# Optimization experiments

Measured on AMD Instinct MI355X. Metric: run time of the kernel, lower is better.

The kernel has to match this reference:

```python
import jax, jax.numpy as jnp
import numpy as np

N, D, K = 131072, 64, 4096


def setup_inputs() -> dict:
    key = jax.random.key(0)
    k1, k2 = jax.random.split(key)
    x = jax.random.normal(k1, (N, D), dtype=jnp.float32)
    embed = jax.random.normal(k2, (K, D), dtype=jnp.float32)
    return {"x": x, "embed": embed}


def reference(x, embed):
    """EuclideanCodebook forward.

    x:     [N, D] flat input vectors
    embed: [K, D] codebook
    Returns (quantize [N,D], embed_ind [N], cluster_size [K], embed_sum [K,D]).
    cluster_size / embed_sum are the one-hot scatter statistics fed to the
    EMA codebook update (embed_onehot.sum(0) and flatten^T @ embed_onehot).
    """
    num_codes = embed.shape[0]
    x2 = jnp.sum(x * x, axis=-1, keepdims=True)               # [N, 1]
    e2 = jnp.sum(embed * embed, axis=-1)                      # [K]
    dist = x2 - 2.0 * (x @ embed.T) + e2[None, :]             # [N, K]
    embed_ind = jnp.argmin(dist, axis=-1)                     # [N]
    quantize = embed[embed_ind]                               # gather [N, D]
    # scatter statistics for EMA update
    cluster_size = jnp.zeros((num_codes,), x.dtype).at[embed_ind].add(1.0)  # [K]
    embed_sum = jax.ops.segment_sum(x, embed_ind, num_segments=num_codes)   # [K, D]
    return quantize, embed_ind, cluster_size, embed_sum
```

## Files before the change

kernel.cpp:

```cpp
#include <hip/hip_runtime.h>

#define N_ROWS 131072
#define DIM 64
#define K_CODES 4096
#define BROWS 256
#define CK 64
#define NCH (K_CODES / CK)
#define EST 72
#define EPS 0.015625f
#define HEPS 0.0078125f

typedef __attribute__((ext_vector_type(8))) short short8;
typedef __attribute__((ext_vector_type(4))) float f32x4;

__device__ inline unsigned short bf16rn(float f) {
    unsigned int u = __float_as_uint(f);
    u += 0x7FFFu + ((u >> 16) & 1u);
    return (unsigned short)(u >> 16);
}
__device__ inline unsigned int fkey(float f) {
    unsigned int u = __float_as_uint(f);
    return (u & 0x80000000u) ? ~u : (u | 0x80000000u);
}

__global__ void pack_kernel(const float* __restrict__ embed,
                            unsigned short* __restrict__ ebf,
                            float* __restrict__ e2,
                            float* __restrict__ e2h,
                            int* __restrict__ cnt,
                            float* __restrict__ cs) {
    const int g = blockIdx.x * blockDim.x + threadIdx.x;
    for (int i = g; i < K_CODES + K_CODES * DIM; i += K_CODES * 16)
        cs[i] = 0.f;
    if (g == 0) *cnt = 0;

    const int code = g >> 4;
    const int w    = g & 15;
    const int half = w >> 3;
    const int d0   = (w & 7) << 3;
    const float* ep = embed + (size_t)code * DIM + d0;
    float4 f0 = *(const float4*)ep;
    float4 f1 = *(const float4*)(ep + 4);
    float wv[8] = {f0.x, f0.y, f0.z, f0.w, f1.x, f1.y, f1.z, f1.w};
    unsigned short o[8];
    float ssq = 0.f;
#pragma unroll
    for (int j = 0; j < 8; ++j) {
        unsigned short hb = bf16rn(wv[j]);
        if (half == 0) {
            o[j] = hb;
            ssq = fmaf(wv[j], wv[j], ssq);
        } else {
            float hf = __uint_as_float(((unsigned int)hb) << 16);
            o[j] = bf16rn(wv[j] - hf);
        }
    }
    *(uint4*)(ebf + (size_t)code * 128 + half * 64 + d0) = *(uint4*)o;
    ssq += __shfl_xor(ssq, 1, 64);
    ssq += __shfl_xor(ssq, 2, 64);
    ssq += __shfl_xor(ssq, 4, 64);
    if (w == 0) {
        e2[code]  = ssq;
        e2h[code] = -0.5f * ssq;
    }
}

__global__ __launch_bounds__(256, 2) void dist_argmin_kernel(
        const float* __restrict__ x, const unsigned short* __restrict__ ebf,
        const float* __restrict__ e2h, int* __restrict__ ind_ws,
        float* __restrict__ ind_out, int* __restrict__ cnt,
        int* __restrict__ list) {
    __shared__ unsigned short esh[2][CK * EST];
    __shared__ unsigned short esl[2][CK * EST];
    __shared__ float e2s[2][CK];

    const int tid  = threadIdx.x;
    const int l15  = tid & 15;
    const int quad = (tid >> 4) & 3;
    const int wave = tid >> 6;
    const int r0w  = blockIdx.x * BROWS + wave * 64;

    const int col = tid >> 2;
    const int dq  = (tid & 3) * 16;

    uint4 sh0, sh1, sl0, sl1;
    float se2 = 0.f;
    {
        const unsigned short* pp = ebf + (size_t)col * 128 + dq;
        sh0 = *(const uint4*)pp;
        sh1 = *(const uint4*)(pp + 8);
        sl0 = *(const uint4*)(pp + 64);
        sl1 = *(const uint4*)(pp + 72);
        if (tid < CK) se2 = e2h[tid];
    }

    short8 ah[4][2], al[4][2];
#pragma unroll
    for (int i = 0; i < 4; ++i)
#pragma unroll
        for (int s = 0; s < 2; ++s) {
            const float* xp = x + (size_t)(r0w + 16 * i + l15) * DIM + 32 * s + 8 * quad;
            float4 f0 = *(const float4*)xp;
            float4 f1 = *(const float4*)(xp + 4);
            float w[8] = {f0.x, f0.y, f0.z, f0.w, f1.x, f1.y, f1.z, f1.w};
            short8 h, l;
#pragma unroll
            for (int j = 0; j < 8; ++j) {
                unsigned short hb = bf16rn(w[j]);
                float hf = __uint_as_float(((unsigned int)hb) << 16);
                h[j] = (short)hb;
                l[j] = (short)bf16rn(w[j] - hf);
            }
            ah[i][s] = h;
            al[i][s] = l;
        }

    *(uint4*)(&esh[0][col * EST + dq])     = sh0;
    *(uint4*)(&esh[0][col * EST + dq + 8]) = sh1;
    *(uint4*)(&esl[0][col * EST + dq])     = sl0;
    *(uint4*)(&esl[0][col * EST + dq + 8]) = sl1;
    if (tid < CK) e2s[0][tid] = se2;

    float s1[16], s2[16];
    int c1[16];
#pragma unroll
    for (int t = 0; t < 16; ++t) { s1[t] = -3.4e38f; s2[t] = -3.4e38f; c1[t] = 0; }

    __syncthreads();

    int cur = 0;
    for (int ch = 0; ch < NCH; ++ch) {
        {
            const int c0n = ((ch + 1) & (NCH - 1)) * CK;
            const unsigned short* pp = ebf + (size_t)(c0n + col) * 128 + dq;
            sh0 = *(const uint4*)pp;
            sh1 = *(const uint4*)(pp + 8);
            sl0 = *(const uint4*)(pp + 64);
            sl1 = *(const uint4*)(pp + 72);
            if (tid < CK) se2 = e2h[c0n + tid];
        }

        const int c0 = ch * CK;

        f32x4 acc[4][4];
#pragma unroll
        for (int j = 0; j < 4; ++j) {
            const float ev = e2s[cur][16 * j + l15];
            const f32x4 iv = {ev, ev, ev, ev};
#pragma unroll
            for (int i = 0; i < 4; ++i) acc[i][j] = iv;
        }

#pragma unroll
        for (int j = 0; j < 4; ++j) {
            const int cb = (16 * j + l15) * EST + 8 * quad;
            short8 bh0 = *(const short8*)(&esh[cur][cb]);
            short8 bh1 = *(const short8*)(&esh[cur][cb + 32]);
            short8 bl0 = *(const short8*)(&esl[cur][cb]);
            short8 bl1 = *(const short8*)(&esl[cur][cb + 32]);
#pragma unroll
            for (int i = 0; i < 4; ++i) {
                f32x4 a = acc[i][j];
                a = __builtin_amdgcn_mfma_f32_16x16x32_bf16(ah[i][0], bh0, a, 0, 0, 0);
                a = __builtin_amdgcn_mfma_f32_16x16x32_bf16(ah[i][1], bh1, a, 0, 0, 0);
                a = __builtin_amdgcn_mfma_f32_16x16x32_bf16(ah[i][0], bl0, a, 0, 0, 0);
                a = __builtin_amdgcn_mfma_f32_16x16x32_bf16(ah[i][1], bl1, a, 0, 0, 0);
                a = __builtin_amdgcn_mfma_f32_16x16x32_bf16(al[i][0], bh0, a, 0, 0, 0);
                a = __builtin_amdgcn_mfma_f32_16x16x32_bf16(al[i][1], bh1, a, 0, 0, 0);
                acc[i][j] = a;
            }
        }

#pragma unroll
        for (int j = 0; j < 4; ++j) {
            const int c = c0 + 16 * j + l15;
#pragma unroll
            for (int i = 0; i < 4; ++i)
#pragma unroll
                for (int r = 0; r < 4; ++r) {
                    float d = acc[i][j][r];
                    const int st = i * 4 + r;
                    bool gt = d > s1[st];
                    s2[st] = fmaxf(fminf(d, s1[st]), s2[st]);
                    c1[st] = gt ? c : c1[st];
                    s1[st] = fmaxf(s1[st], d);
                }
        }

        const int nxt = cur ^ 1;
        *(uint4*)(&esh[nxt][col * EST + dq])     = sh0;
        *(uint4*)(&esh[nxt][col * EST + dq + 8]) = sh1;
        *(uint4*)(&esl[nxt][col * EST + dq])     = sl0;
        *(uint4*)(&esl[nxt][col * EST + dq + 8]) = sl1;
        if (tid < CK) e2s[nxt][tid] = se2;

        __syncthreads();
        cur = nxt;
    }

#pragma unroll
    for (int st = 0; st < 16; ++st) {
#pragma unroll
        for (int m = 1; m < 16; m <<= 1) {
            float os1 = __shfl_xor(s1[st], m, 64);
            float os2 = __shfl_xor(s2[st], m, 64);
            int   oc1 = __shfl_xor(c1[st], m, 64);
            bool take = (os1 > s1[st]) || (os1 == s1[st] && oc1 < c1[st]);
            float loser = take ? s1[st] : os1;
            s2[st] = fmaxf(fmaxf(s2[st], os2), loser);
            if (take) { s1[st] = os1; c1[st] = oc1; }
        }
    }
    if (l15 == 0) {
#pragma unroll
        for (int st = 0; st < 16; ++st) {
            const int i = st >> 2, r = st & 3;
            const int row = r0w + 16 * i + 4 * quad + r;
            ind_ws[row] = c1[st];
            ind_out[row] = (float)c1[st];
            if (s1[st] - s2[st] < HEPS) {
                int p = atomicAdd(cnt, 1);
                list[p] = row;
            }
        }
    }
}

__global__ void refine_kernel(const float* __restrict__ x,
                              const float* __restrict__ embed,
                              const float* __restrict__ e2g,
                              const int* __restrict__ cnt,
                              const int* __restrict__ list,
                              int* __restrict__ ind_ws,
                              float* __restrict__ ind_out) {
    __shared__ float xr[DIM];
    __shared__ unsigned long long red[256];
    const int tid = threadIdx.x;
    const int n = *cnt;
    for (int f = blockIdx.x; f < n; f += gridDim.x) {
        const int row = list[f];
        __syncthreads();
        if (tid < 16)
            ((float4*)xr)[tid] = ((const float4*)(x + (size_t)row * DIM))[tid];
        __syncthreads();
        unsigned long long best = ~0ull;
        for (int c = tid; c < K_CODES; c += 256) {
            const float4* ep = (const float4*)(embed + (size_t)c * DIM);
            float d0 = 0.f, d1 = 0.f, d2 = 0.f, d3 = 0.f;
#pragma unroll
            for (int q = 0; q < 16; ++q) {
                float4 ev = ep[q];
                d0 = fmaf(xr[4 * q + 0], ev.x, d0);
                d1 = fmaf(xr[4 * q + 1], ev.y, d1);
                d2 = fmaf(xr[4 * q + 2], ev.z, d2);
                d3 = fmaf(xr[4 * q + 3], ev.w, d3);
            }
            float sc = fmaf(-2.f, (d0 + d1) + (d2 + d3), e2g[c]);
            unsigned long long key =
                ((unsigned long long)fkey(sc) << 32) | (unsigned int)c;
            if (key < best) best = key;
        }
        red[tid] = best;
        __syncthreads();
        for (int w = 128; w > 0; w >>= 1) {
            if (tid < w && red[tid + w] < red[tid]) red[tid] = red[tid + w];
            __syncthreads();
        }
        if (tid == 0) {
            int k = (int)(red[0] & 0xFFFFFFFFull);
            ind_ws[row] = k;
            ind_out[row] = (float)k;
        }
    }
}

__global__ void scatter_kernel(const float* __restrict__ x,
                               const float* __restrict__ embed,
                               const int* __restrict__ ind,
                               float* __restrict__ quant,
                               float* __restrict__ cs,
                               float* __restrict__ esum) {
    const int t = blockIdx.x * blockDim.x + threadIdx.x;
    const int row = t >> 6;
    const int d = t & 63;
    const int k = ind[row];
    quant[t] = embed[(size_t)k * DIM + d];
    atomicAdd(&esum[(size_t)k * DIM + d], x[t]);
    if (d == 0) atomicAdd(&cs[k], 1.0f);
}

extern "C" void kernel_launch(void* const* d_in, const int* in_sizes, int n_in,
                              void* d_out, int out_size, void* d_ws, size_t ws_size,
                              hipStream_t stream) {
    const float* x     = (const float*)d_in[0];
    const float* embed = (const float*)d_in[1];

    float* out     = (float*)d_out;
    float* quant   = out;
    float* ind_out = out + (size_t)N_ROWS * DIM;
    float* cs      = ind_out + N_ROWS;
    float* esum    = cs + K_CODES;

    float* e2   = (float*)d_ws;
    int* cnt    = (int*)(e2 + K_CODES);
    int* list   = cnt + 4;
    int* ind_ws = list + N_ROWS;
    float* e2h  = (float*)(ind_ws + N_ROWS);

    unsigned short* ebf = (unsigned short*)quant;

    pack_kernel<<<(K_CODES * 16) / 256, 256, 0, stream>>>(
        embed, ebf, e2, e2h, cnt, cs);
    dist_argmin_kernel<<<N_ROWS / BROWS, 256, 0, stream>>>(
        x, ebf, e2h, ind_ws, ind_out, cnt, list);
    refine_kernel<<<512, 256, 0, stream>>>(x, embed, e2, cnt, list, ind_ws, ind_out);
    scatter_kernel<<<(size_t)N_ROWS * DIM / 256, 256, 0, stream>>>(
        x, embed, ind_ws, quant, cs, esum);
}
```

Baseline: 436.8 us.

## Fuse gather and scatter statistics into argmin epilogue with refine-time correction

Moves the quantize gather and the esum/cluster_size atomic accumulation into the tail of the distance/argmin kernel, using the approximate argmin. The refine kernel then subtracts the old code's contribution and adds the new code's contribution for rows whose index changes. The separate scatter launch is dropped, which removes one pass over x and the index array. When the workspace is large enough, the bf16 codebook is moved into workspace instead of the quant buffer. This adds a tail loop inside a heavy kernel, reuses shared memory without a barrier, and depends on the workspace size.

```diff
diff --git a/kernel.cpp b/kernel.cpp
--- a/kernel.cpp
+++ b/kernel.cpp
@@ -67,9 +67,11 @@
 
 __global__ __launch_bounds__(256, 2) void dist_argmin_kernel(
         const float* __restrict__ x, const unsigned short* __restrict__ ebf,
-        const float* __restrict__ e2h, int* __restrict__ ind_ws,
-        float* __restrict__ ind_out, int* __restrict__ cnt,
-        int* __restrict__ list) {
+        const float* __restrict__ e2h, const float* __restrict__ embed,
+        int* __restrict__ ind_ws, float* __restrict__ ind_out,
+        int* __restrict__ cnt, int* __restrict__ list,
+        float* __restrict__ quant, float* __restrict__ cs,
+        float* __restrict__ esum, int fused) {
     __shared__ unsigned short esh[2][CK * EST];
     __shared__ unsigned short esl[2][CK * EST];
     __shared__ float e2s[2][CK];
@@ -224,6 +226,26 @@
             }
         }
     }
+
+    if (fused) {
+        int* li = (int*)&esh[0][0];
+        if (l15 == 0) {
+#pragma unroll
+            for (int st = 0; st < 16; ++st) {
+                const int i = st >> 2, r = st & 3;
+                li[(wave << 6) + 16 * i + 4 * quad + r] = c1[st];
+            }
+        }
+        const int lane = tid & 63;
+        for (int t = 0; t < 64; ++t) {
+            const int k = li[(wave << 6) + t];
+            const size_t row = (size_t)(r0w + t);
+            quant[row * DIM + lane] = embed[(size_t)k * DIM + lane];
+            float xv = x[row * DIM + lane];
+            atomicAdd(&esum[(size_t)k * DIM + lane], xv);
+            if (lane == 0) atomicAdd(&cs[k], 1.0f);
+        }
+    }
 }
 
 __global__ void refine_kernel(const float* __restrict__ x,
@@ -232,7 +254,10 @@
                               const int* __restrict__ cnt,
                               const int* __restrict__ list,
                               int* __restrict__ ind_ws,
-                              float* __restrict__ ind_out) {
+                              float* __restrict__ ind_out,
+                              float* __restrict__ quant,
+                              float* __restrict__ cs,
+                              float* __restrict__ esum, int fused) {
     __shared__ float xr[DIM];
     __shared__ unsigned long long red[256];
     const int tid = threadIdx.x;
@@ -266,10 +291,27 @@
             if (tid < w && red[tid + w] < red[tid]) red[tid] = red[tid + w];
             __syncthreads();
         }
-        if (tid == 0) {
-            int k = (int)(red[0] & 0xFFFFFFFFull);
-            ind_ws[row] = k;
-            ind_out[row] = (float)k;
+        const int k_new = (int)(red[0] & 0xFFFFFFFFull);
+        if (fused) {
+            const int k_old = ind_ws[row];
+            if (k_new != k_old) {
+                if (tid < DIM) {
+                    float xv = xr[tid];
+                    atomicAdd(&esum[(size_t)k_old * DIM + tid], -xv);
+                    atomicAdd(&esum[(size_t)k_new * DIM + tid],  xv);
+                    quant[(size_t)row * DIM + tid] =
+                        embed[(size_t)k_new * DIM + tid];
+                }
+                if (tid == 0) {
+                    atomicAdd(&cs[k_old], -1.f);
+                    atomicAdd(&cs[k_new],  1.f);
+                    ind_ws[row] = k_new;
+                    ind_out[row] = (float)k_new;
+                }
+            }
+        } else if (tid == 0) {
+            ind_ws[row] = k_new;
+            ind_out[row] = (float)k_new;
         }
     }
 }
@@ -306,14 +348,20 @@
     int* list   = cnt + 4;
     int* ind_ws = list + N_ROWS;
     float* e2h  = (float*)(ind_ws + N_ROWS);
-
-    unsigned short* ebf = (unsigned short*)quant;
+    unsigned short* ebf_ws = (unsigned short*)(e2h + K_CODES);
+    const size_t ws_need =
+        (size_t)((char*)(ebf_ws + (size_t)K_CODES * 128) - (char*)d_ws);
+
+    const int fused = (ws_size >= ws_need) ? 1 : 0;
+    unsigned short* ebf = fused ? ebf_ws : (unsigned short*)quant;
 
     pack_kernel<<<(K_CODES * 16) / 256, 256, 0, stream>>>(
         embed, ebf, e2, e2h, cnt, cs);
     dist_argmin_kernel<<<N_ROWS / BROWS, 256, 0, stream>>>(
-        x, ebf, e2h, ind_ws, ind_out, cnt, list);
-    refine_kernel<<<512, 256, 0, stream>>>(x, embed, e2, cnt, list, ind_ws, ind_out);
-    scatter_kernel<<<(size_t)N_ROWS * DIM / 256, 256, 0, stream>>>(
-        x, embed, ind_ws, quant, cs, esum);
-}
+        x, ebf, e2h, embed, ind_ws, ind_out, cnt, list, quant, cs, esum, fused);
+    refine_kernel<<<512, 256, 0, stream>>>(
+        x, embed, e2, cnt, list, ind_ws, ind_out, quant, cs, esum, fused);
+    if (!fused)
+        scatter_kernel<<<(size_t)N_ROWS * DIM / 256, 256, 0, stream>>>(
+            x, embed, ind_ws, quant, cs, esum);
+}
```

Result: faster. 402.5 us (-7.8%).
